# Optimization experiments

Measured on AMD Instinct MI355X. Metric: run time of the kernel, lower is better.

The kernel has to match this reference:

```python
import jax, jax.numpy as jnp
import numpy as np

H_DIM = 2048
N_HEADS = 16
HEAD_DIM = H_DIM // N_HEADS
B, S = 2, 2048


def setup_inputs() -> dict:
    key = jax.random.key(0)
    ks = jax.random.split(key, 10)
    sc = 1.0 / np.sqrt(H_DIM)
    return {
        "X": jax.random.normal(ks[0], (B, S, H_DIM), dtype=jnp.float32),
        "attention_mask": jnp.ones((B, S, S), dtype=jnp.int32),
        "Wq": jax.random.normal(ks[1], (H_DIM, H_DIM), dtype=jnp.float32) * sc,
        "bq": jnp.zeros((H_DIM,), dtype=jnp.float32),
        "Wk": jax.random.normal(ks[2], (H_DIM, H_DIM), dtype=jnp.float32) * sc,
        "bk": jnp.zeros((H_DIM,), dtype=jnp.float32),
        "Wv": jax.random.normal(ks[3], (H_DIM, H_DIM), dtype=jnp.float32) * sc,
        "bv": jnp.zeros((H_DIM,), dtype=jnp.float32),
        "Wo": jax.random.normal(ks[4], (H_DIM, H_DIM), dtype=jnp.float32) * sc,
        "bo": jnp.zeros((H_DIM,), dtype=jnp.float32),
    }


def reference(X, attention_mask, Wq, bq, Wk, bk, Wv, bv, Wo, bo):
    b, s, _ = X.shape
    # QKV projections -> [b, heads, s, head_dim]
    def proj(W, bias):
        y = jnp.einsum("bsd,de->bse", X, W) + bias
        return y.reshape(b, s, N_HEADS, HEAD_DIM).transpose(0, 2, 1, 3)
    Q, K, V = proj(Wq, bq), proj(Wk, bk), proj(Wv, bv)
    # scores [b, h, s, s]
    scores = jnp.einsum("bhqd,bhkd->bhqk", Q, K) / jnp.sqrt(jnp.float32(HEAD_DIM))
    mask = attention_mask[:, None, :, :]  # [b,1,s,s]
    scores = jnp.where(mask == 0, jnp.float32(-jnp.inf), scores)
    attn = jax.nn.softmax(scores, axis=-1)
    # dropout_rate = 0.0 -> no-op
    out = jnp.einsum("bhqk,bhkd->bhqd", attn, V)
    out = out.transpose(0, 2, 1, 3).reshape(b, s, H_DIM)
    return jnp.einsum("bsd,de->bse", out, Wo) + bo
```

## Files before the change

kernel.cpp:

```cpp
#include <hip/hip_runtime.h>
#include <hip/hip_bf16.h>

#define H_DIM 2048
#define N_HEADS 16
#define HEAD_DIM 128
#define BATCH 2
#define SEQ 2048

typedef __bf16 bf16_t;
typedef __bf16 bf16x8 __attribute__((ext_vector_type(8)));
typedef float f32x4 __attribute__((ext_vector_type(4)));

#define MFMA16(a, b, c) __builtin_amdgcn_mfma_f32_16x16x32_bf16((a), (b), (c), 0, 0, 0)

#define GLOAD16(gp, lp) __builtin_amdgcn_global_load_lds( \
    (const __attribute__((address_space(1))) void*)(gp),  \
    (__attribute__((address_space(3))) void*)(lp), 16, 0, 0)

#define WAIT_VM6()  asm volatile("s_waitcnt vmcnt(6)" ::: "memory")
#define WAIT_VM4()  asm volatile("s_waitcnt vmcnt(4)" ::: "memory")
#define WAIT_VM0()  asm volatile("s_waitcnt vmcnt(0)" ::: "memory")
#define RAW_BARRIER() asm volatile("s_barrier" ::: "memory")

__global__ __launch_bounds__(256) void detect_kernel(const unsigned int* __restrict__ X,
                                                     int* __restrict__ flags) {
    __shared__ int cnt[256];
    int t = threadIdx.x;
    int c = 0;
    for (int i = 0; i < 16; i++) {
        unsigned w  = X[t * 16 + i];
        unsigned lo = w & 0xFFFFu;
        unsigned e  = (lo >> 7) & 0xFFu;
        if (lo == 0u || (e >= 100u && e <= 141u)) c++;
    }
    cnt[t] = c;
    __syncthreads();
    for (int s = 128; s > 0; s >>= 1) {
        if (t < s) cnt[t] += cnt[t + s];
        __syncthreads();
    }
    if (t == 0) { flags[0] = (cnt[0] >= 2048) ? 1 : 0; flags[1] = 1; }
}

__global__ __launch_bounds__(256) void maskcheck_kernel(const int* __restrict__ mask,
                                                        int* __restrict__ flags) {
    size_t i = ((size_t)blockIdx.x * 256 + threadIdx.x) * 8;
    const int4* p = (const int4*)(mask + i);
    int4 a = p[0], b = p[1];
    int all = (a.x != 0) & (a.y != 0) & (a.z != 0) & (a.w != 0) &
              (b.x != 0) & (b.y != 0) & (b.z != 0) & (b.w != 0);
    if (!all) atomicAnd(&flags[1], 0);
}

__device__ inline bf16x8 load8(const void* __restrict__ p, size_t idx, int isbf16) {
    if (isbf16) {
        return *(const bf16x8*)((const bf16_t*)p + idx);
    } else {
        const float* f = (const float*)p + idx;
        float4 a = *(const float4*)f;
        float4 b = *(const float4*)(f + 4);
        bf16x8 r;
        r[0] = (bf16_t)a.x; r[1] = (bf16_t)a.y; r[2] = (bf16_t)a.z; r[3] = (bf16_t)a.w;
        r[4] = (bf16_t)b.x; r[5] = (bf16_t)b.y; r[6] = (bf16_t)b.z; r[7] = (bf16_t)b.w;
        return r;
    }
}

__device__ inline float readf(const void* __restrict__ p, int idx, int isbf16) {
    return isbf16 ? (float)((const bf16_t*)p)[idx] : ((const float*)p)[idx];
}

__global__ __launch_bounds__(256) void convert_kernel(const void* __restrict__ X,
                                                      bf16_t* __restrict__ Xb,
                                                      const int* __restrict__ flags) {
    const int isbf16 = flags[0];
    size_t i = ((size_t)blockIdx.x * 256 + threadIdx.x) * 8;
    bf16x8 v = load8(X, i, isbf16);
    *(bf16x8*)(Xb + i) = v;
}

__global__ __launch_bounds__(256) void transpose_kernel(
    const void* __restrict__ W0, const void* __restrict__ W1,
    const void* __restrict__ W2, const void* __restrict__ W3,
    bf16_t* __restrict__ Wts, const int* __restrict__ flags)
{
    const int isbf16 = flags[0];
    const int z = blockIdx.z;
    const void* W = (z == 0) ? W0 : (z == 1) ? W1 : (z == 2) ? W2 : W3;
    bf16_t* out = Wts + (size_t)z * H_DIM * H_DIM;

    __shared__ __attribute__((aligned(16))) bf16_t Ts[64][72];
    const int tid = threadIdx.x;
    const int n0 = blockIdx.x * 64;
    const int k0 = blockIdx.y * 64;

    #pragma unroll
    for (int j = 0; j < 2; j++) {
        int idx = j * 2048 + tid * 8;
        int r = idx >> 6, c = idx & 63;
        bf16x8 v = load8(W, (size_t)(k0 + r) * H_DIM + n0 + c, isbf16);
        *(bf16x8*)(&Ts[r][c]) = v;
    }
    __syncthreads();
    const int wr = tid & 63;
    const int wcg = (tid >> 6) * 8;
    #pragma unroll
    for (int j = 0; j < 2; j++) {
        int wc = wcg + j * 32;
        bf16x8 o;
        #pragma unroll
        for (int u = 0; u < 8; u++) o[u] = Ts[wc + u][wr];
        *(bf16x8*)(&out[(size_t)(n0 + wr) * H_DIM + k0 + wc]) = o;
    }
}

__global__ __launch_bounds__(256, 2) void gemm_qkv_kernel(
    const bf16_t* __restrict__ A, const bf16_t* __restrict__ Wts,
    const void* __restrict__ b0, const void* __restrict__ b1, const void* __restrict__ b2,
    bf16_t* __restrict__ qws, bf16_t* __restrict__ kws, bf16_t* __restrict__ vtws,
    const int* __restrict__ flags)
{
    const int isbf16 = flags[0];
    const int L    = blockIdx.x;
    const int xcd  = L & 7;
    const int j    = L >> 3;
    const int c    = xcd * 6 + (j % 6);
    const int mrow = j / 6;
    const int z    = c >> 4;
    const int m0   = mrow * 256;
    const int n0   = (c & 15) * 128;

    const bf16_t* Wt = Wts + (size_t)z * H_DIM * H_DIM;
    const void* bias = (z == 0) ? b0 : (z == 1) ? b1 : b2;
    bf16_t* dst = (z == 0) ? qws : (z == 1) ? kws : vtws;

    __shared__ __attribute__((aligned(16))) bf16_t As[3][4][256][8];
    __shared__ __attribute__((aligned(16))) bf16_t Bs[3][4][128][8];

    const int tid  = threadIdx.x;
    const int lane = tid & 63;
    const int wid  = tid >> 6;
    const int quad = lane >> 4;
    const int l16  = lane & 15;
    const int wm   = (wid >> 1) * 128;
    const int wn   = (wid & 1) * 64;

    f32x4 acc[8][4] = {};

    auto stage = [&](int k0, int sb) {
        #pragma unroll
        for (int jj = 0; jj < 4; jj++) {
            int slot = jj * 256 + tid;
            int k8 = slot >> 8, row = slot & 255;
            GLOAD16(A + (size_t)(m0 + row) * H_DIM + k0 + k8 * 8,
                    (bf16_t*)(&As[sb][0][0][0]) + slot * 8);
        }
        #pragma unroll
        for (int jj = 0; jj < 2; jj++) {
            int slot = jj * 256 + tid;
            int k8 = slot >> 7, row = slot & 127;
            GLOAD16(Wt + (size_t)(n0 + row) * H_DIM + k0 + k8 * 8,
                    (bf16_t*)(&Bs[sb][0][0][0]) + slot * 8);
        }
    };

    auto body = [&](int it, int bb, int sb, int mode) {
        if (mode == 2) { WAIT_VM0(); } else { WAIT_VM6(); }
        RAW_BARRIER();
        if (mode == 0) stage((it + 2) * 32, sb);
        bf16x8 bfr[4];
        #pragma unroll
        for (int i = 0; i < 4; i++)
            bfr[i] = *(const bf16x8*)(&Bs[bb][quad][wn + i * 16 + l16][0]);
        #pragma unroll
        for (int mi = 0; mi < 8; mi++) {
            bf16x8 af = *(const bf16x8*)(&As[bb][quad][wm + mi * 16 + l16][0]);
            #pragma unroll
            for (int ni = 0; ni < 4; ni++)
                acc[mi][ni] = MFMA16(af, bfr[ni], acc[mi][ni]);
        }
    };

    stage(0, 0);
    stage(32, 1);
    for (int base = 0; base < 60; base += 3) {
        body(base,     0, 2, 0);
        body(base + 1, 1, 0, 0);
        body(base + 2, 2, 1, 0);
    }
    body(60, 0, 2, 0);
    body(61, 1, 0, 0);
    body(62, 2, 1, 1);
    body(63, 0, 0, 2);

    #pragma unroll
    for (int ni = 0; ni < 4; ni++) {
        int col = n0 + wn + ni * 16 + l16;
        int h = col >> 7, d = col & (HEAD_DIM - 1);
        float bv = readf(bias, col, isbf16);
        #pragma unroll
        for (int mi = 0; mi < 8; mi++) {
            int row0 = m0 + wm + mi * 16 + quad * 4;
            int b = row0 >> 11;
            if (z < 2) {
                #pragma unroll
                for (int r = 0; r < 4; r++) {
                    int s = (row0 + r) & (SEQ - 1);
                    dst[((size_t)(b * N_HEADS + h) * SEQ + s) * HEAD_DIM + d] =
                        (bf16_t)(acc[mi][ni][r] + bv);
                }
            } else {
                int s0 = row0 & (SEQ - 1);
                bf16_t o[4];
                #pragma unroll
                for (int r = 0; r < 4; r++) o[r] = (bf16_t)(acc[mi][ni][r] + bv);
                *(unsigned long long*)(&dst[((size_t)(b * N_HEADS + h) * HEAD_DIM + d) * SEQ + s0]) =
                    *(unsigned long long*)o;
            }
        }
    }
}

__global__ __launch_bounds__(256) void gemm_out_kernel(
    const bf16_t* __restrict__ A, const bf16_t* __restrict__ Wt,
    const void* __restrict__ bias, void* __restrict__ C,
    const int* __restrict__ flags)
{
    const int isbf16 = flags[0];
    const int L    = blockIdx.x;
    const int xcd  = L & 7;
    const int j    = L >> 3;
    const int m0   = (j >> 1) * 128;
    const int n0   = (xcd * 2 + (j & 1)) * 128;

    __shared__ __attribute__((aligned(16))) bf16_t As[3][4][128][8];
    __shared__ __attribute__((aligned(16))) bf16_t Bs[3][4][128][8];

    const int tid  = threadIdx.x;
    const int lane = tid & 63;
    const int wid  = tid >> 6;
    const int quad = lane >> 4;
    const int l16  = lane & 15;
    const int wm   = (wid >> 1) * 64;
    const int wn   = (wid & 1) * 64;

    f32x4 acc[4][4] = {};

    auto stage = [&](int k0, int sb) {
        #pragma unroll
        for (int jj = 0; jj < 2; jj++) {
            int slot = jj * 256 + tid;
            int k8 = slot >> 7, row = slot & 127;
            GLOAD16(A  + (size_t)(m0 + row) * H_DIM + k0 + k8 * 8,
                    (bf16_t*)(&As[sb][0][0][0]) + slot * 8);
            GLOAD16(Wt + (size_t)(n0 + row) * H_DIM + k0 + k8 * 8,
                    (bf16_t*)(&Bs[sb][0][0][0]) + slot * 8);
        }
    };

    auto body = [&](int it, int bb, int sb, int mode) {
        if (mode == 2) { WAIT_VM0(); } else { WAIT_VM4(); }
        RAW_BARRIER();
        if (mode == 0) stage((it + 2) * 32, sb);
        bf16x8 af[4], bfr[4];
        #pragma unroll
        for (int i = 0; i < 4; i++) {
            af[i]  = *(const bf16x8*)(&As[bb][quad][wm + i * 16 + l16][0]);
            bfr[i] = *(const bf16x8*)(&Bs[bb][quad][wn + i * 16 + l16][0]);
        }
        #pragma unroll
        for (int mi = 0; mi < 4; mi++)
            #pragma unroll
            for (int ni = 0; ni < 4; ni++)
                acc[mi][ni] = MFMA16(af[mi], bfr[ni], acc[mi][ni]);
    };

    stage(0, 0);
    stage(32, 1);
    for (int base = 0; base < 60; base += 3) {
        body(base,     0, 2, 0);
        body(base + 1, 1, 0, 0);
        body(base + 2, 2, 1, 0);
    }
    body(60, 0, 2, 0);
    body(61, 1, 0, 0);
    body(62, 2, 1, 1);
    body(63, 0, 0, 2);

    #pragma unroll
    for (int ni = 0; ni < 4; ni++) {
        int col = n0 + wn + ni * 16 + l16;
        float bv = readf(bias, col, isbf16);
        #pragma unroll
        for (int mi = 0; mi < 4; mi++) {
            int row0 = m0 + wm + mi * 16 + quad * 4;
            #pragma unroll
            for (int r = 0; r < 4; r++) {
                float v = acc[mi][ni][r] + bv;
                if (isbf16) ((bf16_t*)C)[(size_t)(row0 + r) * H_DIM + col] = (bf16_t)v;
                else        ((float*)C)[(size_t)(row0 + r) * H_DIM + col]  = v;
            }
        }
    }
}

__global__ __launch_bounds__(256) void attn_kernel(
    const bf16_t* __restrict__ Q, const bf16_t* __restrict__ K,
    const bf16_t* __restrict__ Vt, const int* __restrict__ mask,
    const int* __restrict__ flags, bf16_t* __restrict__ ctx)
{
    __shared__ __attribute__((aligned(16))) bf16_t Ks[2][16][64][8];
    __shared__ __attribute__((aligned(16))) bf16_t Vs[2][8][128][8];
    __shared__ __attribute__((aligned(16))) bf16_t Pl[4][16][72];

    const int tid  = threadIdx.x;
    const int lane = tid & 63;
    const int wid  = tid >> 6;
    const int quad = lane >> 4;
    const int l16  = lane & 15;

    const int bh = blockIdx.y;
    const int b  = bh >> 4, h = bh & 15;
    const int q_base = blockIdx.x * 64 + wid * 16;
    const int maskAll = flags[1];

    const bf16_t* Qp = Q  + (size_t)bh * SEQ * HEAD_DIM;
    const bf16_t* Kp = K  + (size_t)bh * SEQ * HEAD_DIM;
    const bf16_t* Vp = Vt + (size_t)bh * HEAD_DIM * SEQ;
    const int*    mp = mask + (size_t)b * SEQ * SEQ;

    bf16x8 qf[4];
    #pragma unroll
    for (int t = 0; t < 4; t++)
        qf[t] = *(const bf16x8*)(Qp + (size_t)(q_base + l16) * HEAD_DIM + t * 32 + quad * 8);

    bf16x8 onesf;
    #pragma unroll
    for (int u = 0; u < 8; u++) onesf[u] = (bf16_t)1.0f;

    const float CS = 0.1275260013f;
    float m_r[4];
    #pragma unroll
    for (int r = 0; r < 4; r++) m_r[r] = -1e30f;
    f32x4 l_acc = {};
    f32x4 o_acc[8] = {};

    auto stage = [&](int kt, int bb) {
        const int key0 = kt * 64;
        #pragma unroll
        for (int jj = 0; jj < 4; jj++) {
            int slot = jj * 256 + tid;
            int krow = slot & 63, k8 = slot >> 6;
            GLOAD16(Kp + (size_t)(key0 + krow) * HEAD_DIM + k8 * 8,
                    (bf16_t*)(&Ks[bb][0][0][0]) + slot * 8);
        }
        #pragma unroll
        for (int jj = 0; jj < 4; jj++) {
            int slot = jj * 256 + tid;
            int d = slot & 127, kq = slot >> 7;
            GLOAD16(Vp + (size_t)d * SEQ + key0 + kq * 8,
                    (bf16_t*)(&Vs[bb][0][0][0]) + slot * 8);
        }
    };

    const int NKT = SEQ / 64;

    auto abody = [&](int kt, int bb) {
        const int key0 = kt * 64;
        __syncthreads();
        if (kt + 1 < NKT) stage(kt + 1, bb ^ 1);

        f32x4 s_acc[4];
        #pragma unroll
        for (int nt = 0; nt < 4; nt++) {
            f32x4 a = {};
            #pragma unroll
            for (int t = 0; t < 4; t++) {
                bf16x8 kf = *(const bf16x8*)(&Ks[bb][t * 4 + quad][nt * 16 + l16][0]);
                a = MFMA16(qf[t], kf, a);
            }
            s_acc[nt] = a;
        }

        float p2[4][4];
        #pragma unroll
        for (int nt = 0; nt < 4; nt++)
            #pragma unroll
            for (int r = 0; r < 4; r++)
                p2[nt][r] = s_acc[nt][r] * CS;

        if (!maskAll) {
            #pragma unroll
            for (int nt = 0; nt < 4; nt++) {
                int key = key0 + nt * 16 + l16;
                #pragma unroll
                for (int r = 0; r < 4; r++) {
                    int q = q_base + quad * 4 + r;
                    if (mp[(size_t)q * SEQ + key] == 0) p2[nt][r] = -1e30f;
                }
            }
        }

        #pragma unroll
        for (int r = 0; r < 4; r++) {
            float tmax = fmaxf(fmaxf(p2[0][r], p2[1][r]), fmaxf(p2[2][r], p2[3][r]));
            #pragma unroll
            for (int off = 1; off < 16; off <<= 1)
                tmax = fmaxf(tmax, __shfl_xor(tmax, off));
            float mnew  = fmaxf(m_r[r], tmax);
            float alpha = exp2f(m_r[r] - mnew);
            m_r[r] = mnew;
            #pragma unroll
            for (int nt = 0; nt < 4; nt++)
                p2[nt][r] = exp2f(p2[nt][r] - mnew);
            l_acc[r] *= alpha;
            #pragma unroll
            for (int dn = 0; dn < 8; dn++)
                o_acc[dn][r] *= alpha;
        }

        #pragma unroll
        for (int nt = 0; nt < 4; nt++)
            #pragma unroll
            for (int r = 0; r < 4; r++)
                Pl[wid][quad * 4 + r][nt * 16 + l16] = (bf16_t)p2[nt][r];

        #pragma unroll
        for (int t = 0; t < 2; t++) {
            bf16x8 pf = *(const bf16x8*)(&Pl[wid][l16][t * 32 + quad * 8]);
            l_acc = MFMA16(pf, onesf, l_acc);
            #pragma unroll
            for (int dn = 0; dn < 8; dn++) {
                bf16x8 vf = *(const bf16x8*)(&Vs[bb][t * 4 + quad][dn * 16 + l16][0]);
                o_acc[dn] = MFMA16(pf, vf, o_acc[dn]);
            }
        }
    };

    stage(0, 0);
    for (int base = 0; base < NKT; base += 2) {
        abody(base, 0);
        abody(base + 1, 1);
    }

    #pragma unroll
    for (int dn = 0; dn < 8; dn++) {
        #pragma unroll
        for (int r = 0; r < 4; r++) {
            int q = q_base + quad * 4 + r;
            int d = dn * 16 + l16;
            float v = o_acc[dn][r] / l_acc[r];
            ctx[((size_t)(b * SEQ + q) * N_HEADS + h) * HEAD_DIM + d] = (bf16_t)v;
        }
    }
}

extern "C" void kernel_launch(void* const* d_in, const int* in_sizes, int n_in,
                              void* d_out, int out_size, void* d_ws, size_t ws_size,
                              hipStream_t stream) {
    const void* X    = d_in[0];
    const int*  mask = (const int*)d_in[1];
    const void* Wq   = d_in[2];
    const void* bq   = d_in[3];
    const void* Wk   = d_in[4];
    const void* bk   = d_in[5];
    const void* Wv   = d_in[6];
    const void* bv   = d_in[7];
    const void* Wo   = d_in[8];
    const void* bo   = d_in[9];

    const size_t NE = (size_t)BATCH * SEQ * H_DIM;
    const size_t NW = (size_t)H_DIM * H_DIM;

    int*    flags = (int*)d_ws;
    bf16_t* Xb    = (bf16_t*)((char*)d_ws + 256);
    bf16_t* Wts   = Xb + NE;
    bf16_t* qws   = Wts + 4 * NW;
    bf16_t* kws   = qws + NE;
    bf16_t* vtws  = kws + NE;
    bf16_t* cws   = vtws + NE;

    detect_kernel<<<1, 256, 0, stream>>>((const unsigned int*)X, flags);
    maskcheck_kernel<<<(BATCH * SEQ * SEQ) / (256 * 8), 256, 0, stream>>>(mask, flags);
    convert_kernel<<<NE / (256 * 8), 256, 0, stream>>>(X, Xb, flags);
    transpose_kernel<<<dim3(32, 32, 4), 256, 0, stream>>>(Wq, Wk, Wv, Wo, Wts, flags);
    gemm_qkv_kernel<<<768, 256, 0, stream>>>(Xb, Wts, bq, bk, bv, qws, kws, vtws, flags);
    attn_kernel<<<dim3(SEQ / 64, BATCH * N_HEADS), 256, 0, stream>>>(
        qws, kws, vtws, mask, flags, cws);
    gemm_out_kernel<<<512, 256, 0, stream>>>(cws, Wts + 3 * NW, bo, d_out, flags);
}
```

Baseline: 647.3 us.

## Switch GEMM and attention pipelines to double buffering with explicit vmcnt waits

Shrinks the QKV and output GEMM LDS staging from triple to double buffering, which lets the QKV GEMM raise its launch bound to 3 blocks per CU. The prefetch of the next K-tile is issued before waiting on the current one. The attention loop replaces __syncthreads with raw barriers and explicit vmcnt waits, so the next tile's loads are overlapped without a full drain. The trade-off is a shallower prefetch distance and an extra barrier per iteration in exchange for higher occupancy, and register pressure may limit the 3-block target.

```diff
diff --git a/kernel.cpp b/kernel.cpp
--- a/kernel.cpp
+++ b/kernel.cpp
@@ -17,6 +17,7 @@
     (const __attribute__((address_space(1))) void*)(gp),  \
     (__attribute__((address_space(3))) void*)(lp), 16, 0, 0)
 
+#define WAIT_VM8()  asm volatile("s_waitcnt vmcnt(8)" ::: "memory")
 #define WAIT_VM6()  asm volatile("s_waitcnt vmcnt(6)" ::: "memory")
 #define WAIT_VM4()  asm volatile("s_waitcnt vmcnt(4)" ::: "memory")
 #define WAIT_VM0()  asm volatile("s_waitcnt vmcnt(0)" ::: "memory")
@@ -114,7 +115,7 @@
     }
 }
 
-__global__ __launch_bounds__(256, 2) void gemm_qkv_kernel(
+__global__ __launch_bounds__(256, 3) void gemm_qkv_kernel(
     const bf16_t* __restrict__ A, const bf16_t* __restrict__ Wts,
     const void* __restrict__ b0, const void* __restrict__ b1, const void* __restrict__ b2,
     bf16_t* __restrict__ qws, bf16_t* __restrict__ kws, bf16_t* __restrict__ vtws,
@@ -134,8 +135,8 @@
     const void* bias = (z == 0) ? b0 : (z == 1) ? b1 : b2;
     bf16_t* dst = (z == 0) ? qws : (z == 1) ? kws : vtws;
 
-    __shared__ __attribute__((aligned(16))) bf16_t As[3][4][256][8];
-    __shared__ __attribute__((aligned(16))) bf16_t Bs[3][4][128][8];
+    __shared__ __attribute__((aligned(16))) bf16_t As[2][4][256][8];
+    __shared__ __attribute__((aligned(16))) bf16_t Bs[2][4][128][8];
 
     const int tid  = threadIdx.x;
     const int lane = tid & 63;
@@ -164,10 +165,11 @@
         }
     };
 
-    auto body = [&](int it, int bb, int sb, int mode) {
-        if (mode == 2) { WAIT_VM0(); } else { WAIT_VM6(); }
-        RAW_BARRIER();
-        if (mode == 0) stage((it + 2) * 32, sb);
+    auto body = [&](int it, int bb, int mode) {
+        RAW_BARRIER();
+        if (mode == 0) stage((it + 1) * 32, bb ^ 1);
+        if (mode == 0) { WAIT_VM6(); } else { WAIT_VM0(); }
+        RAW_BARRIER();
         bf16x8 bfr[4];
         #pragma unroll
         for (int i = 0; i < 4; i++)
@@ -182,16 +184,12 @@
     };
 
     stage(0, 0);
-    stage(32, 1);
-    for (int base = 0; base < 60; base += 3) {
-        body(base,     0, 2, 0);
-        body(base + 1, 1, 0, 0);
-        body(base + 2, 2, 1, 0);
-    }
-    body(60, 0, 2, 0);
-    body(61, 1, 0, 0);
-    body(62, 2, 1, 1);
-    body(63, 0, 0, 2);
+    for (int base = 0; base < 62; base += 2) {
+        body(base,     0, 0);
+        body(base + 1, 1, 0);
+    }
+    body(62, 0, 0);
+    body(63, 1, 1);
 
     #pragma unroll
     for (int ni = 0; ni < 4; ni++) {
@@ -233,8 +231,8 @@
     const int m0   = (j >> 1) * 128;
     const int n0   = (xcd * 2 + (j & 1)) * 128;
 
-    __shared__ __attribute__((aligned(16))) bf16_t As[3][4][128][8];
-    __shared__ __attribute__((aligned(16))) bf16_t Bs[3][4][128][8];
+    __shared__ __attribute__((aligned(16))) bf16_t As[2][4][128][8];
+    __shared__ __attribute__((aligned(16))) bf16_t Bs[2][4][128][8];
 
     const int tid  = threadIdx.x;
     const int lane = tid & 63;
@@ -258,10 +256,11 @@
         }
     };
 
-    auto body = [&](int it, int bb, int sb, int mode) {
-        if (mode == 2) { WAIT_VM0(); } else { WAIT_VM4(); }
-        RAW_BARRIER();
-        if (mode == 0) stage((it + 2) * 32, sb);
+    auto body = [&](int it, int bb, int mode) {
+        RAW_BARRIER();
+        if (mode == 0) stage((it + 1) * 32, bb ^ 1);
+        if (mode == 0) { WAIT_VM4(); } else { WAIT_VM0(); }
+        RAW_BARRIER();
         bf16x8 af[4], bfr[4];
         #pragma unroll
         for (int i = 0; i < 4; i++) {
@@ -276,16 +275,12 @@
     };
 
     stage(0, 0);
-    stage(32, 1);
-    for (int base = 0; base < 60; base += 3) {
-        body(base,     0, 2, 0);
-        body(base + 1, 1, 0, 0);
-        body(base + 2, 2, 1, 0);
-    }
-    body(60, 0, 2, 0);
-    body(61, 1, 0, 0);
-    body(62, 2, 1, 1);
-    body(63, 0, 0, 2);
+    for (int base = 0; base < 62; base += 2) {
+        body(base,     0, 0);
+        body(base + 1, 1, 0);
+    }
+    body(62, 0, 0);
+    body(63, 1, 1);
 
     #pragma unroll
     for (int ni = 0; ni < 4; ni++) {
@@ -365,10 +360,12 @@
 
     const int NKT = SEQ / 64;
 
-    auto abody = [&](int kt, int bb) {
+    auto abody = [&](int kt, int bb, int mode) {
         const int key0 = kt * 64;
-        __syncthreads();
-        if (kt + 1 < NKT) stage(kt + 1, bb ^ 1);
+        RAW_BARRIER();
+        if (mode == 0) stage(kt + 1, bb ^ 1);
+        if (mode == 0) { WAIT_VM8(); } else { WAIT_VM0(); }
+        RAW_BARRIER();
 
         f32x4 s_acc[4];
         #pragma unroll
@@ -438,10 +435,12 @@
     };
 
     stage(0, 0);
-    for (int base = 0; base < NKT; base += 2) {
-        abody(base, 0);
-        abody(base + 1, 1);
-    }
+    for (int base = 0; base < NKT - 2; base += 2) {
+        abody(base,     0, 0);
+        abody(base + 1, 1, 0);
+    }
+    abody(NKT - 2, 0, 0);
+    abody(NKT - 1, 1, 1);
 
     #pragma unroll
     for (int dn = 0; dn < 8; dn++) {
```

Measured after the change: 695.9 us. +7.5%, slower.
